# Performance work log

Measured on AMD Instinct MI355X. Metric: run time of the kernel, lower is better.

## Reference

```python
import jax, jax.numpy as jnp
import numpy as np
import math

B, L, H, NH = 4, 2048, 2048, 16
HD = H // NH  # head_dim = 128
ROPE_BASE = 10000.0


def rotate_half(x):
    x1, x2 = jnp.split(x, 2, axis=-1)
    return jnp.concatenate((-x2, x1), axis=-1)


def rope_cos_sin(seq_len, dim, dtype=jnp.float32):
    inv_freq = 1.0 / (ROPE_BASE ** (jnp.arange(0, dim, 2, dtype=jnp.float32) / dim))
    t = jnp.arange(seq_len, dtype=jnp.float32)
    freqs = jnp.outer(t, inv_freq)              # [L, dim/2]
    emb = jnp.concatenate((freqs, freqs), -1)   # [L, dim]
    return jnp.cos(emb).astype(dtype), jnp.sin(emb).astype(dtype)


def setup_inputs() -> dict:
    key = jax.random.key(0)
    ks = jax.random.split(key, 5)
    x = jax.random.normal(ks[0], (B, L, H), dtype=jnp.float32)
    # causal mask, broadcastable over [B, NH, L, L]; 0 -> masked
    mask = jnp.tril(jnp.ones((L, L), dtype=jnp.int32))[None, None]
    s = 0.02
    Wq = jax.random.normal(ks[1], (H, H), dtype=jnp.float32) * s
    Wk = jax.random.normal(ks[2], (H, H), dtype=jnp.float32) * s
    Wv = jax.random.normal(ks[3], (H, H), dtype=jnp.float32) * s
    Wo = jax.random.normal(ks[4], (H, H), dtype=jnp.float32) * s
    return {"x": x, "mask": mask, "Wq": Wq, "Wk": Wk, "Wv": Wv, "Wo": Wo}


def reference(x, mask, Wq, Wk, Wv, Wo):
    b, l, _ = x.shape
    # nn.Linear: y = x @ W.T (weight shape [out, in])
    q = (x @ Wq.T).reshape(b, l, NH, HD).transpose(0, 2, 1, 3)  # [B,H,L,D]
    k = (x @ Wk.T).reshape(b, l, NH, HD).transpose(0, 2, 1, 3)
    v = (x @ Wv.T).reshape(b, l, NH, HD).transpose(0, 2, 1, 3)
    cos, sin = rope_cos_sin(l, HD, x.dtype)  # [L, D] broadcasts over [B,H,L,D]
    q = q * cos + rotate_half(q) * sin
    k = k * cos + rotate_half(k) * sin
    attn = jnp.einsum("bhqd,bhkd->bhqk", q, k) / math.sqrt(HD)
    attn = jnp.where(mask == 0, jnp.float32(-jnp.inf), attn)
    attn = jax.nn.softmax(attn.astype(jnp.float32), axis=-1).astype(x.dtype)
    out = jnp.einsum("bhqk,bhkd->bhqd", attn, v)
    out = out.transpose(0, 2, 1, 3).reshape(b, l, NH * HD)
    return out @ Wo.T
```

## Files before the change

kernel.cpp:

```cpp
#include <hip/hip_runtime.h>
#include <cstdint>
#include <cmath>

#define B_   4
#define L_   2048
#define H_   2048
#define NH_  16
#define HD_  128
#define ML_  (B_*L_)

using short8 = __attribute__((ext_vector_type(8))) short;
using f32x4  = __attribute__((ext_vector_type(4))) float;
using f32x16 = __attribute__((ext_vector_type(16))) float;
using uint4v = __attribute__((ext_vector_type(4))) unsigned;

__device__ inline short f2bf(float f){
  unsigned u = __builtin_bit_cast(unsigned, f);
  unsigned r = u + 0x7FFFu + ((u >> 16) & 1u);
  return (short)(r >> 16);
}
__device__ inline float bf2f(short s){
  unsigned u = ((unsigned)(unsigned short)s) << 16;
  return __builtin_bit_cast(float, u);
}

#define GLD16(gp, lp) __builtin_amdgcn_global_load_lds(                      \
    (const __attribute__((address_space(1))) void*)(gp),                     \
    (__attribute__((address_space(3))) void*)(lp), 16, 0, 0)

__device__ inline unsigned cvtpk_bf16(float lo, float hi){
  unsigned d;
  asm("v_cvt_pk_bf16_f32 %0, %1, %2" : "=v"(d) : "v"(lo), "v"(hi));
  return d;
}
__device__ inline void permswap32(unsigned &a, unsigned &b){
  asm volatile("v_permlane32_swap_b32 %0, %1" : "+v"(a), "+v"(b));
}
__device__ inline float cross_half_max(float x){
  return fmaxf(x, __shfl_xor(x, 32));
}
__device__ inline float cross_half_add(float x){
  return x + __shfl_xor(x, 32);
}

__global__ void rope_table(float* __restrict__ cosT, float* __restrict__ sinT){
  int idx = blockIdx.x * 256 + threadIdx.x;
  if (idx >= L_ * 64) return;
  int l = idx >> 6, d = idx & 63;
  float invf = powf(10000.0f, -(float)d * (1.0f/64.0f));
  float fr = (float)l * invf;
  cosT[idx] = cosf(fr);
  sinT[idx] = sinf(fr);
}

__global__ __launch_bounds__(256)
void cvt_bf16(const float* __restrict__ in, short* __restrict__ out, int n8){
  int i = blockIdx.x * 256 + threadIdx.x;
  if (i >= n8) return;
  const float4* p = (const float4*)(in + (size_t)i * 8);
  float4 a = p[0], b = p[1];
  short8 s;
  s[0]=f2bf(a.x); s[1]=f2bf(a.y); s[2]=f2bf(a.z); s[3]=f2bf(a.w);
  s[4]=f2bf(b.x); s[5]=f2bf(b.y); s[6]=f2bf(b.z); s[7]=f2bf(b.w);
  *(short8*)(out + (size_t)i * 8) = s;
}

template<int OUT_F32>
__global__ __launch_bounds__(512, 2)
void gemm256_bt(const short* __restrict__ A, const short* __restrict__ Bw,
                void* __restrict__ Cp)
{
  constexpr int K = 2048, N = 2048;
  __shared__ short sA[4][256 * 32];
  __shared__ short sB[4][256 * 32];
  const int tid  = threadIdx.x;
  const int lane = tid & 63;
  const int wave = tid >> 6;
  const int wr = wave >> 2, wc = wave & 3;
  const int ln = lane & 15, g = lane >> 4;

  const int blk = blockIdx.x;
  const int m0 = (blk >> 3) * 256, n0 = (blk & 7) * 256;

  const int u0 = wave * 64 + lane;
  const int u1 = u0 + 512;
  const int r0 = u0 >> 2, c0 = ((u0 & 3) ^ (r0 & 3)) * 8;
  const int r1 = u1 >> 2, c1 = ((u1 & 3) ^ (r1 & 3)) * 8;

  f32x4 acc[8][4];
  #pragma unroll
  for (int m = 0; m < 8; m++)
    #pragma unroll
    for (int n = 0; n < 4; n++) acc[m][n] = {0.f, 0.f, 0.f, 0.f};

#define STAGE256(T) do {                                                     \
    const int _b = (T) & 3; const int _k = (T) * 32;                         \
    GLD16(A  + (size_t)(m0 + r0) * K + _k + c0, &sA[_b][wave * 512]);        \
    GLD16(A  + (size_t)(m0 + r1) * K + _k + c1, &sA[_b][4096 + wave * 512]); \
    GLD16(Bw + (size_t)(n0 + r0) * K + _k + c0, &sB[_b][wave * 512]);        \
    GLD16(Bw + (size_t)(n0 + r1) * K + _k + c1, &sB[_b][4096 + wave * 512]); \
  } while (0)

#define TILE256(T, VMN, PF) do {                                             \
    asm volatile("s_waitcnt vmcnt(" #VMN ")" ::: "memory");                  \
    __builtin_amdgcn_s_barrier();                                            \
    asm volatile("" ::: "memory");                                           \
    const short* _at = &sA[(T) & 3][0];                                      \
    const short* _bt = &sB[(T) & 3][0];                                      \
    short8 af[8], bfr[4];                                                    \
    const int _sl = (g ^ (ln & 3)) * 8;                                      \
    _Pragma("unroll")                                                        \
    for (int m = 0; m < 8; m++)                                              \
      af[m] = *(const short8*)(_at + (wr * 128 + m * 16 + ln) * 32 + _sl);   \
    _Pragma("unroll")                                                        \
    for (int n = 0; n < 4; n++)                                              \
      bfr[n] = *(const short8*)(_bt + (wc * 64 + n * 16 + ln) * 32 + _sl);   \
    if (PF) STAGE256((T) + 3);                                               \
    __builtin_amdgcn_s_setprio(1);                                           \
    _Pragma("unroll")                                                        \
    for (int m = 0; m < 8; m++)                                              \
      _Pragma("unroll")                                                      \
      for (int n = 0; n < 4; n++)                                            \
        acc[m][n] = __builtin_amdgcn_mfma_f32_16x16x32_bf16(af[m], bfr[n],   \
                                                            acc[m][n], 0, 0, 0); \
    __builtin_amdgcn_s_setprio(0);                                           \
  } while (0)

  STAGE256(0); STAGE256(1); STAGE256(2);

  for (int t = 0; t < 61; ++t) TILE256(t, 8, true);
  TILE256(61, 8, false);
  TILE256(62, 4, false);
  TILE256(63, 0, false);

#undef STAGE256
#undef TILE256

  #pragma unroll
  for (int m = 0; m < 8; m++)
    #pragma unroll
    for (int n = 0; n < 4; n++)
      #pragma unroll
      for (int r = 0; r < 4; r++) {
        int row = m0 + wr * 128 + m * 16 + g * 4 + r;
        int col = n0 + wc * 64 + n * 16 + ln;
        float v = acc[m][n][r];
        if constexpr (OUT_F32) ((float*)Cp)[(size_t)row * N + col] = v;
        else                   ((short*)Cp)[(size_t)row * N + col] = f2bf(v);
      }
}

__global__ __launch_bounds__(256)
void rope_apply(short* __restrict__ Qb, short* __restrict__ Kb,
                const float* __restrict__ cosT, const float* __restrict__ sinT)
{
  int idx = blockIdx.x * 256 + threadIdx.x;
  int z = blockIdx.y;
  short* ptr  = z ? Kb : Qb;
  float scale = z ? 1.0f : 0.08838834764831845f;
  int row = idx >> 7;
  int rem = idx & 127;
  int h = rem >> 3, ch = rem & 7;
  int l = row & (L_ - 1);
  short* base = ptr + (size_t)row * H_ + h * HD_ + ch * 8;
  short8 lo = *(short8*)base;
  short8 hi = *(short8*)(base + 64);
  const float* cp = cosT + l * 64 + ch * 8;
  const float* sp = sinT + l * 64 + ch * 8;
  short8 nlo, nhi;
  #pragma unroll
  for (int j = 0; j < 8; j++) {
    float c = cp[j], s = sp[j];
    float x0 = bf2f(lo[j]), x1 = bf2f(hi[j]);
    nlo[j] = f2bf((x0 * c - x1 * s) * scale);
    nhi[j] = f2bf((x1 * c + x0 * s) * scale);
  }
  *(short8*)base        = nlo;
  *(short8*)(base + 64) = nhi;
}

__global__ __launch_bounds__(256)
void transpose_v(const short* __restrict__ Vb, short* __restrict__ VT)
{
  __shared__ short t[64 * 64];
  const int blk = blockIdx.x;
  const int dt = blk & 1, lt = (blk >> 1) & 31, bh = blk >> 6;
  const int b = bh >> 4, h = bh & 15;
  const int l0 = lt * 64, d0 = dt * 64;
  const int tid = threadIdx.x;
  #pragma unroll
  for (int i = 0; i < 2; i++) {
    int u = tid + i * 256;
    int r = u >> 3, c = u & 7;
    short8 v = *(const short8*)(Vb + ((size_t)b * L_ + l0 + r) * H_ + h * HD_ + d0 + c * 8);
    *(short8*)&t[r * 64 + ((c ^ ((r >> 3) & 7)) << 3)] = v;
  }
  __syncthreads();
  #pragma unroll
  for (int i = 0; i < 2; i++) {
    int u = tid + i * 256;
    int d = u >> 3, lc = u & 7;
    short8 o;
    #pragma unroll
    for (int j = 0; j < 8; j++) {
      int l = lc * 8 + j;
      o[j] = t[l * 64 + (((d >> 3) ^ (lc & 7)) << 3) + (d & 7)];
    }
    *(short8*)(VT + ((size_t)bh * HD_ + d0 + d) * L_ + l0 + lc * 8) = o;
  }
}

__global__ __launch_bounds__(512, 2)
void flash_attn(const short* __restrict__ Qb, const short* __restrict__ Kb,
                const short* __restrict__ VT, short* __restrict__ AO)
{
  __shared__ short lds_k[2][64 * 128];
  __shared__ short lds_v[2][128 * 64];
  __shared__ float f_lds[8][32];

  const int blk = blockIdx.x;
  int bh, j;
  if (blk < 256) { bh = blk & 63; j = 7 - (blk >> 6); }
  else           { int u = blk - 256; bh = u & 63; j = 3 - (u >> 6); }
  const int q0 = j * 256;
  const int T  = 4 * j + 4;
  const int h = bh & 15, b = bh >> 4;
  const int tid = threadIdx.x, wave = tid >> 6, lane = tid & 63;
  const int hi = lane >> 5, l31 = lane & 31;
  const size_t rowbase = (size_t)b * L_;
  const int colbase = h * HD_;
  const short* Kbh  = Kb + rowbase * H_ + colbase;
  const short* VTbh = VT + (size_t)bh * HD_ * L_;
  const int qw = q0 + wave * 32;
  const int qabs = qw + l31;

  short8 qf[8];
  {
    const short* qp = Qb + (rowbase + qabs) * H_ + colbase + hi * 8;
    #pragma unroll
    for (int c = 0; c < 8; c++) qf[c] = *(const short8*)(qp + c * 16);
  }

  f32x16 acc_o[4];
  #pragma unroll
  for (int d = 0; d < 4; d++)
    #pragma unroll
    for (int r = 0; r < 16; r++) acc_o[d][r] = 0.f;
  float m_ = -__builtin_inff(), l_ = 0.f;

  auto stage = [&](int k0s, int bufi) {
    #pragma unroll
    for (int i = 0; i < 2; i++) {
      int c = wave * 2 + i;
      {
        int grow = k0s + c * 4 + (lane >> 4);
        const short* gp = Kbh + (size_t)grow * H_ + (((lane & 15) ^ (grow & 7)) * 8);
        GLD16(gp, &lds_k[bufi][c * 512]);
      }
      {
        int d = c * 8 + (lane >> 3);
        const short* gp = VTbh + (size_t)d * L_ + k0s + (((lane & 7) ^ (d & 7)) * 8);
        GLD16(gp, &lds_v[bufi][c * 512]);
      }
    }
  };

  stage(0, 0);
  __syncthreads();

  for (int t = 0; t < T; ++t) {
    const int k0 = t * 64;
    if (t + 1 < T) stage((t + 1) * 64, (t + 1) & 1);
    const short* kb_ = lds_k[t & 1];
    const short* vb_ = lds_v[t & 1];

    if (k0 <= qw + 31) {
      f32x16 p0, p1;
      #pragma unroll
      for (int r = 0; r < 16; r++) { p0[r] = 0.f; p1[r] = 0.f; }
      __builtin_amdgcn_s_setprio(1);
      #pragma unroll
      for (int c = 0; c < 8; c++) {
        int ch = (c * 2 + hi) ^ (l31 & 7);
        short8 kf0 = *(const short8*)(kb_ + l31 * 128 + ch * 8);
        short8 kf1 = *(const short8*)(kb_ + (32 + l31) * 128 + ch * 8);
        p0 = __builtin_amdgcn_mfma_f32_32x32x16_bf16(kf0, qf[c], p0, 0, 0, 0);
        p1 = __builtin_amdgcn_mfma_f32_32x32x16_bf16(kf1, qf[c], p1, 0, 0, 0);
      }
      __builtin_amdgcn_s_setprio(0);

      if (k0 + 63 > qw) {
        #pragma unroll
        for (int r = 0; r < 16; r++) {
          int kvl = (r & 3) + 8 * (r >> 2) + 4 * hi;
          if (k0 + kvl > qabs)      p0[r] = -__builtin_inff();
          if (k0 + 32 + kvl > qabs) p1[r] = -__builtin_inff();
        }
      }

      float mt = p0[0];
      #pragma unroll
      for (int r = 1; r < 16; r++) mt = fmaxf(mt, p0[r]);
      #pragma unroll
      for (int r = 0; r < 16; r++) mt = fmaxf(mt, p1[r]);
      mt = cross_half_max(mt);
      float mnew = fmaxf(m_, mt);
      float f = __expf(m_ - mnew);
      m_ = mnew;
      float ls = 0.f;
      #pragma unroll
      for (int r = 0; r < 16; r++) { p0[r] = __expf(p0[r] - mnew); ls += p0[r]; }
      #pragma unroll
      for (int r = 0; r < 16; r++) { p1[r] = __expf(p1[r] - mnew); ls += p1[r]; }
      ls = cross_half_add(ls);
      l_ = l_ * f + ls;

      if (lane < 32) f_lds[wave][lane] = f;
      f32x4 fr[4];
      #pragma unroll
      for (int i = 0; i < 4; i++)
        fr[i] = *(const f32x4*)&f_lds[wave][i * 8 + hi * 4];
      #pragma unroll
      for (int d = 0; d < 4; d++)
        #pragma unroll
        for (int r = 0; r < 16; r++) acc_o[d][r] *= fr[r >> 2][r & 3];

      __builtin_amdgcn_s_setprio(1);
      #pragma unroll
      for (int ks = 0; ks < 4; ks++) {
        const f32x16 &pp = (ks < 2) ? p0 : p1;
        const int kk = (ks & 1) * 8;
        unsigned a0 = cvtpk_bf16(pp[kk + 0], pp[kk + 1]);
        unsigned b0 = cvtpk_bf16(pp[kk + 4], pp[kk + 5]);
        permswap32(a0, b0);
        unsigned a1 = cvtpk_bf16(pp[kk + 2], pp[kk + 3]);
        unsigned b1 = cvtpk_bf16(pp[kk + 6], pp[kk + 7]);
        permswap32(a1, b1);
        uint4v w; w[0] = a0; w[1] = a1; w[2] = b0; w[3] = b1;
        short8 af = __builtin_bit_cast(short8, w);
        #pragma unroll
        for (int db = 0; db < 4; db++) {
          int d  = db * 32 + l31;
          int ch = (ks * 2 + hi) ^ (d & 7);
          short8 vf = *(const short8*)(vb_ + d * 64 + ch * 8);
          acc_o[db] = __builtin_amdgcn_mfma_f32_32x32x16_bf16(af, vf, acc_o[db], 0, 0, 0);
        }
      }
      __builtin_amdgcn_s_setprio(0);
    }
    __syncthreads();
  }

  if (lane < 32) f_lds[wave][lane] = 1.0f / l_;
  f32x4 lr[4];
  #pragma unroll
  for (int i = 0; i < 4; i++)
    lr[i] = *(const f32x4*)&f_lds[wave][i * 8 + hi * 4];
  #pragma unroll
  for (int db = 0; db < 4; db++)
    #pragma unroll
    for (int r = 0; r < 16; r++) {
      int row = qw + (r & 3) + 8 * (r >> 2) + 4 * hi;
      AO[(rowbase + row) * H_ + colbase + db * 32 + l31] =
          f2bf(acc_o[db][r] * lr[r >> 2][r & 3]);
    }
}

extern "C" void kernel_launch(void* const* d_in, const int* in_sizes, int n_in,
                              void* d_out, int out_size, void* d_ws, size_t ws_size,
                              hipStream_t stream)
{
  const float* x  = (const float*)d_in[0];
  const float* Wq = (const float*)d_in[2];
  const float* Wk = (const float*)d_in[3];
  const float* Wv = (const float*)d_in[4];
  const float* Wo = (const float*)d_in[5];
  float* out = (float*)d_out;

  char* ws = (char*)d_ws;
  const size_t SZ = (size_t)ML_ * H_ * sizeof(short);
  short* Qb = (short*)(ws);
  short* Kb = (short*)(ws + SZ);
  short* Vb = (short*)(ws + 2 * SZ);
  short* xb = (short*)(ws + 3 * SZ);
  short* VT = xb;
  short* AO = Vb;
  short* Wb = (short*)(ws + 4 * SZ);
  float* cosT = (float*)(ws + 4 * SZ + (size_t)H_ * H_ * sizeof(short));
  float* sinT = cosT + (size_t)L_ * 64;

  rope_table<<<512, 256, 0, stream>>>(cosT, sinT);

  cvt_bf16<<<ML_ * H_ / 8 / 256, 256, 0, stream>>>(x, xb, ML_ * H_ / 8);

  cvt_bf16<<<H_ * H_ / 8 / 256, 256, 0, stream>>>(Wq, Wb, H_ * H_ / 8);
  gemm256_bt<0><<<256, 512, 0, stream>>>(xb, Wb, Qb);
  cvt_bf16<<<H_ * H_ / 8 / 256, 256, 0, stream>>>(Wk, Wb, H_ * H_ / 8);
  gemm256_bt<0><<<256, 512, 0, stream>>>(xb, Wb, Kb);
  cvt_bf16<<<H_ * H_ / 8 / 256, 256, 0, stream>>>(Wv, Wb, H_ * H_ / 8);
  gemm256_bt<0><<<256, 512, 0, stream>>>(xb, Wb, Vb);

  transpose_v<<<64 * 32 * 2, 256, 0, stream>>>(Vb, VT);

  rope_apply<<<dim3(ML_ * NH_ * 8 / 256, 2), 256, 0, stream>>>(Qb, Kb, cosT, sinT);

  flash_attn<<<512, 512, 0, stream>>>(Qb, Kb, VT, AO);

  cvt_bf16<<<H_ * H_ / 8 / 256, 256, 0, stream>>>(Wo, Wb, H_ * H_ / 8);
  gemm256_bt<1><<<256, 512, 0, stream>>>(AO, Wb, out);
}
```

Measured before the change: 462.1 us.

## Fuse QKV projections, refine LDS swizzles, and skip unneeded softmax rescales

Converts the three projection weights in one kernel and runs a single 768-block GEMM that writes Q, K and V. This removes two launches and fills the GPU better than three 256-block GEMMs. It also adds an extra XOR term to the LDS swizzle in both the GEMM and flash attention to cut bank conflicts. Attention now skips the output rescale when the running max rises by at most 8, trading exactness of the max shift for fewer multiplies. The fused path only runs when the workspace is large enough, and the lazy rescale risks overflow in exp if score ranges are large.

```diff
diff --git a/kernel.cpp b/kernel.cpp
--- a/kernel.cpp
+++ b/kernel.cpp
@@ -65,10 +65,28 @@
   *(short8*)(out + (size_t)i * 8) = s;
 }
 
-template<int OUT_F32>
+__global__ __launch_bounds__(256)
+void cvt_w3(const float* __restrict__ W0, const float* __restrict__ W1,
+            const float* __restrict__ W2, short* __restrict__ out){
+  int i = blockIdx.x * 256 + threadIdx.x;
+  const int per = H_ * H_ / 8;
+  const float* src; int j;
+  if (i < per)            { src = W0; j = i; }
+  else if (i < 2 * per)   { src = W1; j = i - per; }
+  else                    { src = W2; j = i - 2 * per; }
+  const float4* p = (const float4*)(src + (size_t)j * 8);
+  float4 a = p[0], b = p[1];
+  short8 s;
+  s[0]=f2bf(a.x); s[1]=f2bf(a.y); s[2]=f2bf(a.z); s[3]=f2bf(a.w);
+  s[4]=f2bf(b.x); s[5]=f2bf(b.y); s[6]=f2bf(b.z); s[7]=f2bf(b.w);
+  *(short8*)(out + (size_t)i * 8) = s;
+}
+
+template<int QKV, int OUT_F32>
 __global__ __launch_bounds__(512, 2)
 void gemm256_bt(const short* __restrict__ A, const short* __restrict__ Bw,
-                void* __restrict__ Cp)
+                void* __restrict__ C0, void* __restrict__ C1,
+                void* __restrict__ C2)
 {
   constexpr int K = 2048, N = 2048;
   __shared__ short sA[4][256 * 32];
@@ -80,12 +98,16 @@
   const int ln = lane & 15, g = lane >> 4;
 
   const int blk = blockIdx.x;
-  const int m0 = (blk >> 3) * 256, n0 = (blk & 7) * 256;
+  int n_t, m_t;
+  if constexpr (QKV) { int i = blk >> 3; n_t = (blk & 7) + 8 * (i >> 5); m_t = i & 31; }
+  else               { n_t = blk & 7;    m_t = blk >> 3; }
+  const int m0 = m_t * 256;
+  const int nb0 = n_t * 256;
 
   const int u0 = wave * 64 + lane;
   const int u1 = u0 + 512;
-  const int r0 = u0 >> 2, c0 = ((u0 & 3) ^ (r0 & 3)) * 8;
-  const int r1 = u1 >> 2, c1 = ((u1 & 3) ^ (r1 & 3)) * 8;
+  const int r0 = u0 >> 2, c0 = (((u0 & 3) ^ (r0 & 3) ^ ((r0 >> 2) & 3))) * 8;
+  const int r1 = u1 >> 2, c1 = (((u1 & 3) ^ (r1 & 3) ^ ((r1 >> 2) & 3))) * 8;
 
   f32x4 acc[8][4];
   #pragma unroll
@@ -97,8 +119,8 @@
     const int _b = (T) & 3; const int _k = (T) * 32;                         \
     GLD16(A  + (size_t)(m0 + r0) * K + _k + c0, &sA[_b][wave * 512]);        \
     GLD16(A  + (size_t)(m0 + r1) * K + _k + c1, &sA[_b][4096 + wave * 512]); \
-    GLD16(Bw + (size_t)(n0 + r0) * K + _k + c0, &sB[_b][wave * 512]);        \
-    GLD16(Bw + (size_t)(n0 + r1) * K + _k + c1, &sB[_b][4096 + wave * 512]); \
+    GLD16(Bw + (size_t)(nb0 + r0) * K + _k + c0, &sB[_b][wave * 512]);       \
+    GLD16(Bw + (size_t)(nb0 + r1) * K + _k + c1, &sB[_b][4096 + wave * 512]);\
   } while (0)
 
 #define TILE256(T, VMN, PF) do {                                             \
@@ -108,7 +130,7 @@
     const short* _at = &sA[(T) & 3][0];                                      \
     const short* _bt = &sB[(T) & 3][0];                                      \
     short8 af[8], bfr[4];                                                    \
-    const int _sl = (g ^ (ln & 3)) * 8;                                      \
+    const int _sl = (g ^ (ln & 3) ^ ((ln >> 2) & 3)) * 8;                    \
     _Pragma("unroll")                                                        \
     for (int m = 0; m < 8; m++)                                              \
       af[m] = *(const short8*)(_at + (wr * 128 + m * 16 + ln) * 32 + _sl);   \
@@ -136,6 +158,12 @@
 #undef STAGE256
 #undef TILE256
 
+  void* Cp; int cb;
+  if constexpr (QKV) {
+    int w = n_t >> 3;
+    Cp = (w == 0) ? C0 : (w == 1) ? C1 : C2;
+    cb = (n_t & 7) * 256;
+  } else { Cp = C0; cb = nb0; }
   #pragma unroll
   for (int m = 0; m < 8; m++)
     #pragma unroll
@@ -143,7 +171,7 @@
       #pragma unroll
       for (int r = 0; r < 4; r++) {
         int row = m0 + wr * 128 + m * 16 + g * 4 + r;
-        int col = n0 + wc * 64 + n * 16 + ln;
+        int col = cb + wc * 64 + n * 16 + ln;
         float v = acc[m][n][r];
         if constexpr (OUT_F32) ((float*)Cp)[(size_t)row * N + col] = v;
         else                   ((short*)Cp)[(size_t)row * N + col] = f2bf(v);
@@ -233,6 +261,7 @@
   const short* VTbh = VT + (size_t)bh * HD_ * L_;
   const int qw = q0 + wave * 32;
   const int qabs = qw + l31;
+  const int fsw = (l31 & 7) ^ ((l31 >> 3) & 3);
 
   short8 qf[8];
   {
@@ -253,13 +282,15 @@
     for (int i = 0; i < 2; i++) {
       int c = wave * 2 + i;
       {
-        int grow = k0s + c * 4 + (lane >> 4);
-        const short* gp = Kbh + (size_t)grow * H_ + (((lane & 15) ^ (grow & 7)) * 8);
+        int rt = c * 4 + (lane >> 4);
+        int cg = (lane & 15) ^ (rt & 7) ^ ((rt >> 3) & 3);
+        const short* gp = Kbh + (size_t)(k0s + rt) * H_ + cg * 8;
         GLD16(gp, &lds_k[bufi][c * 512]);
       }
       {
-        int d = c * 8 + (lane >> 3);
-        const short* gp = VTbh + (size_t)d * L_ + k0s + (((lane & 7) ^ (d & 7)) * 8);
+        int rd = c * 8 + (lane >> 3);
+        int cg = (lane & 7) ^ (rd & 7) ^ ((rd >> 3) & 3);
+        const short* gp = VTbh + (size_t)rd * L_ + k0s + cg * 8;
         GLD16(gp, &lds_v[bufi][c * 512]);
       }
     }
@@ -281,7 +312,7 @@
       __builtin_amdgcn_s_setprio(1);
       #pragma unroll
       for (int c = 0; c < 8; c++) {
-        int ch = (c * 2 + hi) ^ (l31 & 7);
+        int ch = (c * 2 + hi) ^ fsw;
         short8 kf0 = *(const short8*)(kb_ + l31 * 128 + ch * 8);
         short8 kf1 = *(const short8*)(kb_ + (32 + l31) * 128 + ch * 8);
         p0 = __builtin_amdgcn_mfma_f32_32x32x16_bf16(kf0, qf[c], p0, 0, 0, 0);
@@ -304,26 +335,28 @@
       #pragma unroll
       for (int r = 0; r < 16; r++) mt = fmaxf(mt, p1[r]);
       mt = cross_half_max(mt);
-      float mnew = fmaxf(m_, mt);
-      float f = __expf(m_ - mnew);
-      m_ = mnew;
+      if (!__all(mt <= m_ + 8.0f)) {
+        float mnew = fmaxf(m_, mt);
+        float f = __expf(m_ - mnew);
+        m_ = mnew;
+        l_ *= f;
+        if (lane < 32) f_lds[wave][lane] = f;
+        f32x4 fr[4];
+        #pragma unroll
+        for (int i = 0; i < 4; i++)
+          fr[i] = *(const f32x4*)&f_lds[wave][i * 8 + hi * 4];
+        #pragma unroll
+        for (int d = 0; d < 4; d++)
+          #pragma unroll
+          for (int r = 0; r < 16; r++) acc_o[d][r] *= fr[r >> 2][r & 3];
+      }
       float ls = 0.f;
       #pragma unroll
-      for (int r = 0; r < 16; r++) { p0[r] = __expf(p0[r] - mnew); ls += p0[r]; }
-      #pragma unroll
-      for (int r = 0; r < 16; r++) { p1[r] = __expf(p1[r] - mnew); ls += p1[r]; }
+      for (int r = 0; r < 16; r++) { p0[r] = __expf(p0[r] - m_); ls += p0[r]; }
+      #pragma unroll
+      for (int r = 0; r < 16; r++) { p1[r] = __expf(p1[r] - m_); ls += p1[r]; }
       ls = cross_half_add(ls);
-      l_ = l_ * f + ls;
-
-      if (lane < 32) f_lds[wave][lane] = f;
-      f32x4 fr[4];
-      #pragma unroll
-      for (int i = 0; i < 4; i++)
-        fr[i] = *(const f32x4*)&f_lds[wave][i * 8 + hi * 4];
-      #pragma unroll
-      for (int d = 0; d < 4; d++)
-        #pragma unroll
-        for (int r = 0; r < 16; r++) acc_o[d][r] *= fr[r >> 2][r & 3];
+      l_ += ls;
 
       __builtin_amdgcn_s_setprio(1);
       #pragma unroll
@@ -341,7 +374,7 @@
         #pragma unroll
         for (int db = 0; db < 4; db++) {
           int d  = db * 32 + l31;
-          int ch = (ks * 2 + hi) ^ (d & 7);
+          int ch = (ks * 2 + hi) ^ fsw;
           short8 vf = *(const short8*)(vb_ + d * 64 + ch * 8);
           acc_o[db] = __builtin_amdgcn_mfma_f32_32x32x16_bf16(af, vf, acc_o[db], 0, 0, 0);
         }
@@ -385,20 +418,27 @@
   short* xb = (short*)(ws + 3 * SZ);
   short* VT = xb;
   short* AO = Vb;
-  short* Wb = (short*)(ws + 4 * SZ);
-  float* cosT = (float*)(ws + 4 * SZ + (size_t)H_ * H_ * sizeof(short));
+  float* cosT = (float*)(ws + 4 * SZ);
   float* sinT = cosT + (size_t)L_ * 64;
+  short* Wb = (short*)(ws + 4 * SZ + (size_t)(1 << 20));
+  const size_t NEED_FUSED = 4 * SZ + (1 << 20) + (size_t)3 * H_ * H_ * sizeof(short);
+  const bool fused = ws_size >= NEED_FUSED;
 
   rope_table<<<512, 256, 0, stream>>>(cosT, sinT);
 
   cvt_bf16<<<ML_ * H_ / 8 / 256, 256, 0, stream>>>(x, xb, ML_ * H_ / 8);
 
-  cvt_bf16<<<H_ * H_ / 8 / 256, 256, 0, stream>>>(Wq, Wb, H_ * H_ / 8);
-  gemm256_bt<0><<<256, 512, 0, stream>>>(xb, Wb, Qb);
-  cvt_bf16<<<H_ * H_ / 8 / 256, 256, 0, stream>>>(Wk, Wb, H_ * H_ / 8);
-  gemm256_bt<0><<<256, 512, 0, stream>>>(xb, Wb, Kb);
-  cvt_bf16<<<H_ * H_ / 8 / 256, 256, 0, stream>>>(Wv, Wb, H_ * H_ / 8);
-  gemm256_bt<0><<<256, 512, 0, stream>>>(xb, Wb, Vb);
+  if (fused) {
+    cvt_w3<<<3 * H_ * H_ / 8 / 256, 256, 0, stream>>>(Wq, Wk, Wv, Wb);
+    gemm256_bt<1, 0><<<768, 512, 0, stream>>>(xb, Wb, Qb, Kb, Vb);
+  } else {
+    cvt_bf16<<<H_ * H_ / 8 / 256, 256, 0, stream>>>(Wq, Wb, H_ * H_ / 8);
+    gemm256_bt<0, 0><<<256, 512, 0, stream>>>(xb, Wb, Qb, Qb, Qb);
+    cvt_bf16<<<H_ * H_ / 8 / 256, 256, 0, stream>>>(Wk, Wb, H_ * H_ / 8);
+    gemm256_bt<0, 0><<<256, 512, 0, stream>>>(xb, Wb, Kb, Kb, Kb);
+    cvt_bf16<<<H_ * H_ / 8 / 256, 256, 0, stream>>>(Wv, Wb, H_ * H_ / 8);
+    gemm256_bt<0, 0><<<256, 512, 0, stream>>>(xb, Wb, Vb, Vb, Vb);
+  }
 
   transpose_v<<<64 * 32 * 2, 256, 0, stream>>>(Vb, VT);
 
@@ -407,5 +447,5 @@
   flash_attn<<<512, 512, 0, stream>>>(Qb, Kb, VT, AO);
 
   cvt_bf16<<<H_ * H_ / 8 / 256, 256, 0, stream>>>(Wo, Wb, H_ * H_ / 8);
-  gemm256_bt<1><<<256, 512, 0, stream>>>(AO, Wb, out);
-}
+  gemm256_bt<0, 1><<<256, 512, 0, stream>>>(AO, Wb, out, out, out);
+}
```

Result: faster. 446.3 us (-3.4%).
